# Performance work log

Measured on AMD Instinct MI355X. Metric: run time of the kernel, lower is better.

## Reference

```python
import jax, jax.numpy as jnp
import numpy as np

HEADS = 8
DIM_HEAD = 64


def setup_inputs() -> dict:
    key = jax.random.key(0)
    ks = jax.random.split(key, 6)
    b, n, d = 4, 2048, 512
    inner = HEADS * DIM_HEAD  # 512
    return {
        "x": jax.random.normal(ks[0], (b, n, d), dtype=jnp.float32),
        "W_v": jax.random.normal(ks[1], (d, inner), dtype=jnp.float32) * 0.02,
        "W_sigma": jax.random.normal(ks[2], (d, HEADS), dtype=jnp.float32) * 0.02,
        "b_sigma": jax.random.normal(ks[3], (HEADS,), dtype=jnp.float32) * 0.02,
        "W_out": jax.random.normal(ks[4], (inner, d), dtype=jnp.float32) * 0.02,
        "b_out": jax.random.normal(ks[5], (d,), dtype=jnp.float32) * 0.02,
    }


def reference(x, W_v, W_sigma, b_sigma, W_out, b_out):
    b, n, d = x.shape
    h, dh = HEADS, DIM_HEAD
    # |i - j| distance matrix (linspace(1,n,n) differences == arange differences)
    pos = jnp.arange(n, dtype=x.dtype)
    dist = jnp.abs(pos[:, None] - pos[None, :])  # (n, n)
    # per-query-row sigma: (b, h, n)
    sigma = jax.nn.sigmoid(jnp.einsum("bnd,dh->bhn", x, W_sigma) + b_sigma[None, :, None])
    denom = jnp.exp(sigma) + 1.0  # (b, h, n)
    # prior[b,h,i,j] = softmax_j( -|i-j| / (exp(sigma[b,h,i]) + 1) )
    prior = jax.nn.softmax(-dist[None, None, :, :] / denom[..., None], axis=-1)  # (b,h,n,n)
    v = (x @ W_v).reshape(b, n, h, dh).transpose(0, 2, 1, 3)  # (b,h,n,dh)
    out = jnp.einsum("bhij,bhjd->bhid", prior, v)  # (b,h,n,dh)
    out = out.transpose(0, 2, 1, 3).reshape(b, n, h * dh)
    return out @ W_out + b_out
```

## Files before the change

kernel.cpp:

```cpp
#include <hip/hip_runtime.h>
#include <hip/hip_bf16.h>

#define B 4
#define N 2048
#define D 512
#define H 8
#define DH 64
#define ROWS (B * N)
#define WIN 64
#define LPAD 64
#define RPAD 128
#define SEG (LPAD + N + RPAD)
#define LDV (B * SEG)

using bf16x8 = __attribute__((ext_vector_type(8))) short;
using f32x4  = __attribute__((ext_vector_type(4))) float;

static __device__ __forceinline__ unsigned short f2bf(float f) {
    unsigned u = __builtin_bit_cast(unsigned, f);
    u += 0x7fffu + ((u >> 16) & 1u);
    return (unsigned short)(u >> 16);
}
static __device__ __forceinline__ unsigned pack2(float a, float b) {
    return (unsigned)f2bf(a) | ((unsigned)f2bf(b) << 16);
}

__global__ __launch_bounds__(256) void prep_fused(const float* __restrict__ x,
                                                  const float* __restrict__ Ws,
                                                  const float* __restrict__ bs,
                                                  const float* __restrict__ Wv,
                                                  const float* __restrict__ Wo,
                                                  unsigned short* __restrict__ xbf,
                                                  float* __restrict__ l2rbuf,
                                                  unsigned short* __restrict__ WvT,
                                                  unsigned short* __restrict__ WoT,
                                                  unsigned short* __restrict__ Vt) {
    __shared__ float tile[64][65];
    const int bx = blockIdx.x;

    if (bx < 2048) {
        const int wid = threadIdx.x >> 6, lane = threadIdx.x & 63;
        const int row = bx * 4 + wid;
        const float* xr = x + (size_t)row * D + lane * 8;
        const float4 a = *reinterpret_cast<const float4*>(xr);
        const float4 c = *reinterpret_cast<const float4*>(xr + 4);
        float v[8] = {a.x, a.y, a.z, a.w, c.x, c.y, c.z, c.w};

        uint4 o;
        o.x = pack2(v[0], v[1]); o.y = pack2(v[2], v[3]);
        o.z = pack2(v[4], v[5]); o.w = pack2(v[6], v[7]);
        *reinterpret_cast<uint4*>(xbf + (size_t)row * D + lane * 8) = o;

        const float4* Ws4 = reinterpret_cast<const float4*>(Ws);
        f32x4 alo = (f32x4)0.0f, ahi = (f32x4)0.0f;
#pragma unroll
        for (int j = 0; j < 8; j++) {
            const int e = lane * 8 + j;
            const float4 wl = Ws4[e * 2], wh = Ws4[e * 2 + 1];
            alo[0] += v[j] * wl.x; alo[1] += v[j] * wl.y; alo[2] += v[j] * wl.z; alo[3] += v[j] * wl.w;
            ahi[0] += v[j] * wh.x; ahi[1] += v[j] * wh.y; ahi[2] += v[j] * wh.z; ahi[3] += v[j] * wh.w;
        }
#pragma unroll
        for (int off = 1; off < 64; off <<= 1) {
#pragma unroll
            for (int c2 = 0; c2 < 4; c2++) {
                alo[c2] += __shfl_xor(alo[c2], off, 64);
                ahi[c2] += __shfl_xor(ahi[c2], off, 64);
            }
        }
        if (lane < 8) {
            const int h = lane;
            const float acc = (h < 4) ? alo[h] : ahi[h - 4];
            const float z = acc + bs[h];
            const float sig = 1.0f / (1.0f + expf(-z));
            const float s = expf(sig) + 1.0f;
            l2rbuf[(size_t)row * H + h] = -1.4426950408889634f / s;
        }
        return;
    }

    if (bx < 2176) {
        const int idx = bx - 2048;
        const bool second = idx >= 64;
        const int id2 = idx & 63;
        const float* src = second ? Wo : Wv;
        unsigned short* dst = second ? WoT : WvT;
        const int n0 = (id2 & 7) * 64, k0 = (id2 >> 3) * 64;
        const int tr = threadIdx.x >> 4, tc = threadIdx.x & 15;
#pragma unroll
        for (int it = 0; it < 4; it++) {
            const int r = it * 16 + tr;
            const float4 v = *reinterpret_cast<const float4*>(&src[(size_t)(k0 + r) * 512 + n0 + tc * 4]);
            tile[r][tc * 4 + 0] = v.x; tile[r][tc * 4 + 1] = v.y;
            tile[r][tc * 4 + 2] = v.z; tile[r][tc * 4 + 3] = v.w;
        }
        __syncthreads();
#pragma unroll
        for (int it = 0; it < 4; it++) {
            const int r = it * 16 + tr;
            ushort4 o;
            o.x = f2bf(tile[tc * 4 + 0][r]); o.y = f2bf(tile[tc * 4 + 1][r]);
            o.z = f2bf(tile[tc * 4 + 2][r]); o.w = f2bf(tile[tc * 4 + 3][r]);
            *reinterpret_cast<ushort4*>(&dst[(size_t)(n0 + r) * 512 + k0 + tc * 4]) = o;
        }
        return;
    }

    {
        const int idx = bx - 2176;
        for (int t = idx * 256 + threadIdx.x; t < 512 * 4 * 24; t += 64 * 256) {
            const int c = t % 24;
            const int bb = (t / 24) & 3;
            const int row = t / 96;
            const int col = (c < 8) ? bb * SEG + c * 8 : bb * SEG + LPAD + N + (c - 8) * 8;
            *reinterpret_cast<uint4*>(Vt + (size_t)row * LDV + col) = uint4{0, 0, 0, 0};
        }
    }
}

#define GBM 128
#define GBN 128
#define GBK 64

template <int MODE>
__global__ __launch_bounds__(256) void gemm_bf16(const unsigned short* __restrict__ A,
                                                 const unsigned short* __restrict__ Bt,
                                                 const float* __restrict__ bias,
                                                 void* __restrict__ Cout,
                                                 int M, int Nn, int K, int ldc) {
    __shared__ unsigned short As[2][GBM][GBK];
    __shared__ unsigned short Bs[2][GBN][GBK];
    const int tid = threadIdx.x;
    const int lane = tid & 63, wid = tid >> 6;
    const int wr = wid >> 1, wc = wid & 1;
    const int bm = blockIdx.y, bn = blockIdx.x;
    const int fr = lane & 15, kg = lane >> 4;

    f32x4 acc[4][4] = {};

    const unsigned short* Ab = A + (size_t)bm * GBM * K;
    const unsigned short* Bb = Bt + (size_t)bn * GBN * K;
    const int r8 = tid >> 3, c8 = (tid & 7) * 8;

    auto stage = [&](int buf, int k0) {
#pragma unroll
        for (int it = 0; it < 4; it++) {
            const unsigned short* g = Ab + (size_t)(it * 32 + r8) * K + k0 + c8;
            __builtin_amdgcn_global_load_lds(
                (const __attribute__((address_space(1))) void*)g,
                (__attribute__((address_space(3))) void*)&As[buf][it * 32 + r8][c8], 16, 0, 0);
        }
#pragma unroll
        for (int it = 0; it < 4; it++) {
            const unsigned short* g = Bb + (size_t)(it * 32 + r8) * K + k0 + c8;
            __builtin_amdgcn_global_load_lds(
                (const __attribute__((address_space(1))) void*)g,
                (__attribute__((address_space(3))) void*)&Bs[buf][it * 32 + r8][c8], 16, 0, 0);
        }
    };

    stage(0, 0);
    __syncthreads();
    int cur = 0;
    for (int k0 = 0; k0 < K; k0 += GBK) {
        if (k0 + GBK < K) stage(cur ^ 1, k0 + GBK);
#pragma unroll
        for (int ks = 0; ks < 2; ks++) {
            bf16x8 af[4], bfr[4];
#pragma unroll
            for (int m = 0; m < 4; m++)
                af[m] = *reinterpret_cast<const bf16x8*>(&As[cur][wr * 64 + m * 16 + fr][ks * 32 + kg * 8]);
#pragma unroll
            for (int n = 0; n < 4; n++)
                bfr[n] = *reinterpret_cast<const bf16x8*>(&Bs[cur][wc * 64 + n * 16 + fr][ks * 32 + kg * 8]);
#pragma unroll
            for (int m = 0; m < 4; m++)
#pragma unroll
                for (int n = 0; n < 4; n++)
                    acc[m][n] = __builtin_amdgcn_mfma_f32_16x16x32_bf16(af[m], bfr[n], acc[m][n], 0, 0, 0);
        }
        __syncthreads();
        cur ^= 1;
    }

#pragma unroll
    for (int n = 0; n < 4; n++) {
        const int col = bn * GBN + wc * 64 + n * 16 + fr;
        const float bv = (MODE == 0 && bias) ? bias[col] : 0.0f;
        const int cp = (MODE == 2) ? ((col >> 11) * SEG + LPAD + (col & 2047)) : col;
#pragma unroll
        for (int m = 0; m < 4; m++) {
            const int row0 = bm * GBM + wr * 64 + m * 16 + kg * 4;
#pragma unroll
            for (int j = 0; j < 4; j++) {
                const int row = row0 + j;
                if (MODE == 0)
                    ((float*)Cout)[(size_t)row * ldc + col] = acc[m][n][j] + bv;
                else
                    ((unsigned short*)Cout)[(size_t)row * ldc + cp] = f2bf(acc[m][n][j]);
            }
        }
    }
}

__global__ __launch_bounds__(256) void attn_mfma(const unsigned short* __restrict__ Vt,
                                                 const float* __restrict__ l2rbuf,
                                                 unsigned short* __restrict__ O) {
    const int wid = threadIdx.x >> 6;
    const int lane = threadIdx.x & 63;
    const int fr = lane & 15, kg = lane >> 4;
    const int gi = blockIdx.x * 4 + wid;
    const int iblk = gi & 127;
    const int bh = gi >> 7;
    const int h = bh & 7;
    const int b = bh >> 3;
    const int i0 = iblk * 16;

    const int i = i0 + fr;
    const float l2rf = l2rbuf[((size_t)(b * N + i)) * H + h];

    const unsigned short* Vrow = Vt + (size_t)(h * DH + fr) * LDV + (size_t)b * SEG + i0 + kg * 8;

    f32x4 acc[4] = {};

#pragma unroll
    for (int s = 0; s < 5; s++) {
        const float basef = (float)(s * 32 + kg * 8 - WIN - fr);
        float wv[8];
#pragma unroll
        for (int j2 = 0; j2 < 8; j2++)
            wv[j2] = __builtin_amdgcn_exp2f(l2rf * __builtin_fabsf(basef + (float)j2));
        uint4 uw;
        uw.x = pack2(wv[0], wv[1]); uw.y = pack2(wv[2], wv[3]);
        uw.z = pack2(wv[4], wv[5]); uw.w = pack2(wv[6], wv[7]);
        const bf16x8 pB = __builtin_bit_cast(bf16x8, uw);
#pragma unroll
        for (int sub = 0; sub < 4; sub++) {
            const bf16x8 aF = *reinterpret_cast<const bf16x8*>(Vrow + (size_t)(sub * 16) * LDV + s * 32);
            acc[sub] = __builtin_amdgcn_mfma_f32_16x16x32_bf16(aF, pB, acc[sub], 0, 0, 0);
        }
    }

    const float rr = __builtin_amdgcn_exp2f(l2rf);
    const float inv1mr = 1.0f / (1.0f - rr);
    const float rl = __builtin_amdgcn_exp2f(l2rf * (float)(i + 1));
    const float rg = __builtin_amdgcn_exp2f(l2rf * (float)(N - i));
    const float invz = 1.0f / (1.0f + (2.0f * rr - rl - rg) * inv1mr);

    unsigned short* orow = O + ((size_t)(b * N + i)) * D + h * DH + kg * 4;
#pragma unroll
    for (int sub = 0; sub < 4; sub++) {
        uint2 o;
        o.x = pack2(acc[sub][0] * invz, acc[sub][1] * invz);
        o.y = pack2(acc[sub][2] * invz, acc[sub][3] * invz);
        *reinterpret_cast<uint2*>(orow + sub * 16) = o;
    }
}

extern "C" void kernel_launch(void* const* d_in, const int* in_sizes, int n_in,
                              void* d_out, int out_size, void* d_ws, size_t ws_size,
                              hipStream_t stream) {
    const float* x      = (const float*)d_in[0];
    const float* W_v    = (const float*)d_in[1];
    const float* W_sig  = (const float*)d_in[2];
    const float* b_sig  = (const float*)d_in[3];
    const float* W_out  = (const float*)d_in[4];
    const float* b_out  = (const float*)d_in[5];
    float* out = (float*)d_out;

    char* ws = (char*)d_ws;
    unsigned short* Vt   = (unsigned short*)ws;
    unsigned short* xbf  = (unsigned short*)(ws + (size_t)9  * 1024 * 1024);
    unsigned short* WvT  = (unsigned short*)(ws + (size_t)17 * 1024 * 1024);
    unsigned short* WoT  = (unsigned short*)(ws + (size_t)17 * 1024 * 1024 + 524288);
    float*          l2r  = (float*)(ws + (size_t)18 * 1024 * 1024);
    unsigned short* attnOut = xbf;

    prep_fused<<<2240, 256, 0, stream>>>(x, W_sig, b_sig, W_v, W_out,
                                         xbf, l2r, WvT, WoT, Vt);

    {
        dim3 grid(ROWS / GBN, 512 / GBM);
        gemm_bf16<2><<<grid, 256, 0, stream>>>(WvT, xbf, nullptr, Vt, 512, ROWS, D, LDV);
    }
    attn_mfma<<<B * H * (N / 16) / 4, 256, 0, stream>>>(Vt, l2r, attnOut);
    {
        dim3 grid(D / GBN, ROWS / GBM);
        gemm_bf16<0><<<grid, 256, 0, stream>>>(attnOut, WoT, b_out, out, ROWS, D, D, D);
    }
}
```

Before: 68.13 us.

## Use 32x32x16 MFMA tiles in banded attention and swizzle output GEMM blocks

```diff
diff --git a/kernel.cpp b/kernel.cpp
--- a/kernel.cpp
+++ b/kernel.cpp
@@ -15,6 +15,7 @@
 
 using bf16x8 = __attribute__((ext_vector_type(8))) short;
 using f32x4  = __attribute__((ext_vector_type(4))) float;
+using f32x16 = __attribute__((ext_vector_type(16))) float;
 
 static __device__ __forceinline__ unsigned short f2bf(float f) {
     unsigned u = __builtin_bit_cast(unsigned, f);
@@ -133,7 +134,13 @@
     const int tid = threadIdx.x;
     const int lane = tid & 63, wid = tid >> 6;
     const int wr = wid >> 1, wc = wid & 1;
-    const int bm = blockIdx.y, bn = blockIdx.x;
+    int bm, bn;
+    if (MODE == 0) {
+        const int swz = (blockIdx.x & 7) * 32 + (blockIdx.x >> 3);
+        bm = swz >> 2; bn = swz & 3;
+    } else {
+        bm = blockIdx.y; bn = blockIdx.x;
+    }
     const int fr = lane & 15, kg = lane >> 4;
 
     f32x4 acc[4][4] = {};
@@ -208,38 +215,38 @@
                                                  unsigned short* __restrict__ O) {
     const int wid = threadIdx.x >> 6;
     const int lane = threadIdx.x & 63;
-    const int fr = lane & 15, kg = lane >> 4;
+    const int il = lane & 31, hi = lane >> 5;
     const int gi = blockIdx.x * 4 + wid;
-    const int iblk = gi & 127;
-    const int bh = gi >> 7;
+    const int iblk = gi & 63;
+    const int bh = gi >> 6;
     const int h = bh & 7;
     const int b = bh >> 3;
-    const int i0 = iblk * 16;
-
-    const int i = i0 + fr;
+    const int i0 = iblk * 32;
+
+    const int i = i0 + il;
     const float l2rf = l2rbuf[((size_t)(b * N + i)) * H + h];
 
-    const unsigned short* Vrow = Vt + (size_t)(h * DH + fr) * LDV + (size_t)b * SEG + i0 + kg * 8;
-
-    f32x4 acc[4] = {};
-
-#pragma unroll
-    for (int s = 0; s < 5; s++) {
-        const float basef = (float)(s * 32 + kg * 8 - WIN - fr);
+    const unsigned short* Va = Vt + (size_t)(h * DH + il) * LDV + (size_t)b * SEG + i0 + hi * 8;
+
+    f32x16 acc0 = (f32x16)0.0f, acc1 = (f32x16)0.0f;
+    __builtin_amdgcn_s_setprio(1);
+#pragma unroll
+    for (int ks = 0; ks < 10; ks++) {
+        const float jb = (float)(ks * 16 + hi * 8 - WIN - il);
         float wv[8];
 #pragma unroll
-        for (int j2 = 0; j2 < 8; j2++)
-            wv[j2] = __builtin_amdgcn_exp2f(l2rf * __builtin_fabsf(basef + (float)j2));
+        for (int e = 0; e < 8; e++)
+            wv[e] = __builtin_amdgcn_exp2f(l2rf * __builtin_fabsf(jb + (float)e));
         uint4 uw;
         uw.x = pack2(wv[0], wv[1]); uw.y = pack2(wv[2], wv[3]);
         uw.z = pack2(wv[4], wv[5]); uw.w = pack2(wv[6], wv[7]);
         const bf16x8 pB = __builtin_bit_cast(bf16x8, uw);
-#pragma unroll
-        for (int sub = 0; sub < 4; sub++) {
-            const bf16x8 aF = *reinterpret_cast<const bf16x8*>(Vrow + (size_t)(sub * 16) * LDV + s * 32);
-            acc[sub] = __builtin_amdgcn_mfma_f32_16x16x32_bf16(aF, pB, acc[sub], 0, 0, 0);
-        }
-    }
+        const bf16x8 a0 = *reinterpret_cast<const bf16x8*>(Va + (size_t)ks * 16);
+        const bf16x8 a1 = *reinterpret_cast<const bf16x8*>(Va + (size_t)32 * LDV + (size_t)ks * 16);
+        acc0 = __builtin_amdgcn_mfma_f32_32x32x16_bf16(a0, pB, acc0, 0, 0, 0);
+        acc1 = __builtin_amdgcn_mfma_f32_32x32x16_bf16(a1, pB, acc1, 0, 0, 0);
+    }
+    __builtin_amdgcn_s_setprio(0);
 
     const float rr = __builtin_amdgcn_exp2f(l2rf);
     const float inv1mr = 1.0f / (1.0f - rr);
@@ -247,13 +254,16 @@
     const float rg = __builtin_amdgcn_exp2f(l2rf * (float)(N - i));
     const float invz = 1.0f / (1.0f + (2.0f * rr - rl - rg) * inv1mr);
 
-    unsigned short* orow = O + ((size_t)(b * N + i)) * D + h * DH + kg * 4;
-#pragma unroll
-    for (int sub = 0; sub < 4; sub++) {
-        uint2 o;
-        o.x = pack2(acc[sub][0] * invz, acc[sub][1] * invz);
-        o.y = pack2(acc[sub][2] * invz, acc[sub][3] * invz);
-        *reinterpret_cast<uint2*>(orow + sub * 16) = o;
+    unsigned short* orow = O + ((size_t)(b * N + i)) * D + h * DH + 4 * hi;
+#pragma unroll
+    for (int q = 0; q < 4; q++) {
+        uint2 o0, o1;
+        o0.x = pack2(acc0[4 * q + 0] * invz, acc0[4 * q + 1] * invz);
+        o0.y = pack2(acc0[4 * q + 2] * invz, acc0[4 * q + 3] * invz);
+        *reinterpret_cast<uint2*>(orow + 8 * q) = o0;
+        o1.x = pack2(acc1[4 * q + 0] * invz, acc1[4 * q + 1] * invz);
+        o1.y = pack2(acc1[4 * q + 2] * invz, acc1[4 * q + 3] * invz);
+        *reinterpret_cast<uint2*>(orow + 32 + 8 * q) = o1;
     }
 }
 
@@ -283,9 +293,6 @@
         dim3 grid(ROWS / GBN, 512 / GBM);
         gemm_bf16<2><<<grid, 256, 0, stream>>>(WvT, xbf, nullptr, Vt, 512, ROWS, D, LDV);
     }
-    attn_mfma<<<B * H * (N / 16) / 4, 256, 0, stream>>>(Vt, l2r, attnOut);
-    {
-        dim3 grid(D / GBN, ROWS / GBM);
-        gemm_bf16<0><<<grid, 256, 0, stream>>>(attnOut, WoT, b_out, out, ROWS, D, D, D);
-    }
-}
+    attn_mfma<<<B * H * (N / 32) / 4, 256, 0, stream>>>(Vt, l2r, attnOut);
+    gemm_bf16<0><<<256, 256, 0, stream>>>(attnOut, WoT, b_out, out, ROWS, D, D, D);
+}
```

New measurement: 66.78 us. 2.0% less time.
